# Kernel optimization log

Hardware: AMD Instinct MI355X
Metric: run time of the kernel (lower is better)

The kernel has to match this reference:

```python
import jax, jax.numpy as jnp
import numpy as np

D_MODEL, N_LEVELS, N_HEADS, N_POINTS = 256, 3, 8, 2
HEAD_DIM = D_MODEL // N_HEADS
SPATIAL_SHAPES = np.array([[100, 100], [50, 50], [25, 25]], dtype=np.int32)
LEN_IN = int((SPATIAL_SHAPES[:, 0] * SPATIAL_SHAPES[:, 1]).sum())  # 13125
BS, NQ = 16, 900


def setup_inputs() -> dict:
    key = jax.random.key(0)
    ks = jax.random.split(key, 12)
    s = 1.0 / np.sqrt(D_MODEL)
    return {
        "query": jax.random.normal(ks[0], (BS, NQ, N_LEVELS, D_MODEL), jnp.float32),
        "reference_points": jax.random.uniform(ks[1], (BS, NQ, N_LEVELS, 2), jnp.float32),
        "input_flatten": jax.random.normal(ks[2], (BS, LEN_IN, D_MODEL), jnp.float32),
        "input_spatial_shapes": jnp.asarray(SPATIAL_SHAPES),
        "W_value": jax.random.normal(ks[3], (D_MODEL, D_MODEL), jnp.float32) * s,
        "b_value": jnp.zeros((D_MODEL,), jnp.float32),
        "W_off": jax.random.normal(ks[4], (D_MODEL, N_HEADS * N_LEVELS * N_POINTS * 2), jnp.float32) * s * 0.1,
        "b_off": jax.random.normal(ks[5], (N_HEADS * N_LEVELS * N_POINTS * 2,), jnp.float32) * 0.5,
        "W_attn": jax.random.normal(ks[6], (D_MODEL, N_HEADS * N_LEVELS * N_POINTS), jnp.float32) * s,
        "b_attn": jnp.zeros((N_HEADS * N_LEVELS * N_POINTS,), jnp.float32),
        "W_out": jax.random.normal(ks[7], (D_MODEL, D_MODEL), jnp.float32) * s,
        "b_out": jnp.zeros((D_MODEL,), jnp.float32),
    }


def _bilinear_sample(v, loc, H, W):
    """v: (bs, nh, H*W, hd); loc in [0,1]: (bs, nh, N, 2). Zero-pad out of range."""
    hd = v.shape[-1]
    x = loc[..., 0] * W - 0.5
    y = loc[..., 1] * H - 0.5
    x0 = jnp.floor(x)
    y0 = jnp.floor(y)
    out = jnp.zeros(x.shape + (hd,), v.dtype)
    for dx in (0, 1):
        for dy in (0, 1):
            xi = x0 + dx
            yi = y0 + dy
            wgt = (1.0 - jnp.abs(x - xi)) * (1.0 - jnp.abs(y - yi))
            valid = (xi >= 0) & (xi <= W - 1) & (yi >= 0) & (yi <= H - 1)
            xi_c = jnp.clip(xi, 0, W - 1).astype(jnp.int32)
            yi_c = jnp.clip(yi, 0, H - 1).astype(jnp.int32)
            idx = yi_c * W + xi_c  # (bs, nh, N)
            idx = jnp.broadcast_to(idx[..., None], idx.shape + (hd,))
            g = jnp.take_along_axis(v, idx, axis=2)  # (bs, nh, N, hd)
            out = out + g * (wgt * valid.astype(wgt.dtype))[..., None]
    return out


def reference(query, reference_points, input_flatten, input_spatial_shapes,
              W_value, b_value, W_off, b_off, W_attn, b_attn, W_out, b_out):
    bs, nq, fl, _ = query.shape
    shapes = np.asarray(input_spatial_shapes)  # static pyramid shapes

    # value projection: (bs, Len, nh, hd)
    value = (input_flatten @ W_value + b_value).reshape(bs, -1, N_HEADS, HEAD_DIM)

    # sampling offsets: (bs, nq, fl, nh, nl, np, 2)
    offsets = (query @ W_off + b_off).reshape(bs, nq, fl, N_HEADS, N_LEVELS, N_POINTS, 2)
    # attention weights softmax over (nl*np): (bs, nq, fl, nh, nl, np)
    attn = (query @ W_attn + b_attn).reshape(bs, nq, fl, N_HEADS, N_LEVELS * N_POINTS)
    attn = jax.nn.softmax(attn, axis=-1).reshape(bs, nq, fl, N_HEADS, N_LEVELS, N_POINTS)

    # normalized sampling locations: ref + offset / (W_l, H_l)
    normalizer = jnp.asarray(shapes[:, ::-1], jnp.float32)  # (nl, 2) = (W, H)
    loc = reference_points[:, :, :, None, None, None, :] + offsets / normalizer[None, None, None, None, :, None, :]

    splits = np.cumsum([h * w for h, w in shapes])[:-1]
    value_list = jnp.split(value, splits, axis=1)

    out = jnp.zeros((bs, N_HEADS, nq, fl, HEAD_DIM), value.dtype)
    for lvl, (H, W) in enumerate(shapes):
        H, W = int(H), int(W)
        v = jnp.transpose(value_list[lvl], (0, 2, 1, 3))  # (bs, nh, H*W, hd)
        loc_l = jnp.transpose(loc[:, :, :, :, lvl], (0, 3, 1, 2, 4, 5))  # (bs, nh, nq, fl, np, 2)
        loc_flat = loc_l.reshape(bs, N_HEADS, nq * fl * N_POINTS, 2)
        sampled = _bilinear_sample(v, loc_flat, H, W).reshape(bs, N_HEADS, nq, fl, N_POINTS, HEAD_DIM)
        w = jnp.transpose(attn[:, :, :, :, lvl], (0, 3, 1, 2, 4))  # (bs, nh, nq, fl, np)
        out = out + jnp.einsum("bhqfpd,bhqfp->bhqfd", sampled, w)

    out = jnp.transpose(out, (0, 2, 3, 1, 4)).reshape(bs, nq, fl, D_MODEL)
    return out @ W_out + b_out
```

## Files before the change

### kernel.cpp

```cpp
#include <hip/hip_runtime.h>
#include <math.h>

#define D_MODEL   256
#define N_HEADS   8
#define HEAD_DIM  32
#define N_LEVELS  3
#define N_POINTS  2
#define BS        16
#define NQ        900
#define LEN_IN    13125
#define M_Q       (BS * NQ * N_LEVELS)
#define M_V       (BS * LEN_IN)
#define NCAT      144
#define NCATP     192

typedef _Float16 f16x8 __attribute__((ext_vector_type(8)));
typedef _Float16 f16x4 __attribute__((ext_vector_type(4)));
typedef float f32x4 __attribute__((ext_vector_type(4)));

__global__ __launch_bounds__(256) void convert_weight_kernel(
    const float* __restrict__ W, _Float16* __restrict__ Wth,
    _Float16* __restrict__ Wtl, int N, int Npad) {
  const int idx = blockIdx.x * 256 + threadIdx.x;
  if (idx >= Npad * 256) return;
  const int n = idx >> 8;
  const int k = idx & 255;
  const float v = (n < N) ? W[(size_t)k * N + n] : 0.0f;
  const _Float16 h = (_Float16)v;
  Wth[idx] = h;
  Wtl[idx] = (_Float16)(v - (float)h);
}

__global__ __launch_bounds__(256) void convert_cat_kernel(
    const float* __restrict__ Woff, const float* __restrict__ Wattn,
    const float* __restrict__ boff, const float* __restrict__ battn,
    _Float16* __restrict__ Wth, _Float16* __restrict__ Wtl,
    float* __restrict__ bcat) {
  const int idx = blockIdx.x * 256 + threadIdx.x;
  if (idx >= NCATP * 256) return;
  const int n = idx >> 8;
  const int k = idx & 255;
  float v = 0.0f;
  if (n < 96) v = Woff[(size_t)k * 96 + n];
  else if (n < NCAT) v = Wattn[(size_t)k * 48 + (n - 96)];
  const _Float16 h = (_Float16)v;
  Wth[idx] = h;
  Wtl[idx] = (_Float16)(v - (float)h);
  if (idx < NCAT) bcat[idx] = (idx < 96) ? boff[idx] : battn[idx - 96];
}

template <int FC>
__global__ __launch_bounds__(256) void gemm2_kernel(
    const float* __restrict__ A, const _Float16* __restrict__ Bth,
    const _Float16* __restrict__ Btl, const float* __restrict__ bias,
    float* __restrict__ C, int M, int N) {
  constexpr int K = 256;
  constexpr int LDA = 40;
  __shared__ _Float16 Ah[2][64][LDA];
  __shared__ _Float16 Al[2][64][LDA];

  const int tid = threadIdx.x;
  const int wid = tid >> 6;
  const int lane = tid & 63;
  const int bm = blockIdx.x * 64;
  const int rsel = lane & 15;
  const int khi = (lane >> 4) * 8;

  const int arow = tid >> 3;
  const int ak = (tid & 7) * 4;
  const bool g0 = (bm + arow) < M;
  const bool g1 = (bm + arow + 32) < M;
  const float* ap0 = A + (size_t)(bm + arow) * K + ak;
  const float* ap1 = ap0 + (size_t)32 * K;

  const _Float16* bhp = Bth + (size_t)(wid * FC * 16 + rsel) * K + khi;
  const _Float16* blp = Btl + (size_t)(wid * FC * 16 + rsel) * K + khi;

  f32x4 acc[4][FC];
#pragma unroll
  for (int fr = 0; fr < 4; ++fr)
#pragma unroll
    for (int fc = 0; fc < FC; ++fc) acc[fr][fc] = (f32x4)0.0f;

  const float4 z4 = make_float4(0.f, 0.f, 0.f, 0.f);

  float4 a0 = g0 ? *reinterpret_cast<const float4*>(ap0) : z4;
  float4 a1 = g1 ? *reinterpret_cast<const float4*>(ap1) : z4;
  f16x8 bh[FC], bl[FC];
#pragma unroll
  for (int fc = 0; fc < FC; ++fc) {
    bh[fc] = *reinterpret_cast<const f16x8*>(bhp + (size_t)fc * 16 * K);
    bl[fc] = *reinterpret_cast<const f16x8*>(blp + (size_t)fc * 16 * K);
  }
  {
    f16x4 h0, l0, h1, l1;
    h0[0] = (_Float16)a0.x; l0[0] = (_Float16)(a0.x - (float)h0[0]);
    h0[1] = (_Float16)a0.y; l0[1] = (_Float16)(a0.y - (float)h0[1]);
    h0[2] = (_Float16)a0.z; l0[2] = (_Float16)(a0.z - (float)h0[2]);
    h0[3] = (_Float16)a0.w; l0[3] = (_Float16)(a0.w - (float)h0[3]);
    h1[0] = (_Float16)a1.x; l1[0] = (_Float16)(a1.x - (float)h1[0]);
    h1[1] = (_Float16)a1.y; l1[1] = (_Float16)(a1.y - (float)h1[1]);
    h1[2] = (_Float16)a1.z; l1[2] = (_Float16)(a1.z - (float)h1[2]);
    h1[3] = (_Float16)a1.w; l1[3] = (_Float16)(a1.w - (float)h1[3]);
    *reinterpret_cast<f16x4*>(&Ah[0][arow][ak]) = h0;
    *reinterpret_cast<f16x4*>(&Al[0][arow][ak]) = l0;
    *reinterpret_cast<f16x4*>(&Ah[0][arow + 32][ak]) = h1;
    *reinterpret_cast<f16x4*>(&Al[0][arow + 32][ak]) = l1;
  }
  __syncthreads();

#pragma unroll 2
  for (int s = 0; s < 8; ++s) {
    const int cur = s & 1;
    float4 na0 = z4, na1 = z4;
    f16x8 nbh[FC], nbl[FC];
    if (s < 7) {
      na0 = g0 ? *reinterpret_cast<const float4*>(ap0 + (s + 1) * 32) : z4;
      na1 = g1 ? *reinterpret_cast<const float4*>(ap1 + (s + 1) * 32) : z4;
#pragma unroll
      for (int fc = 0; fc < FC; ++fc) {
        nbh[fc] = *reinterpret_cast<const f16x8*>(
            bhp + (size_t)fc * 16 * K + (s + 1) * 32);
        nbl[fc] = *reinterpret_cast<const f16x8*>(
            blp + (size_t)fc * 16 * K + (s + 1) * 32);
      }
    }
    f16x8 afh[4], afl[4];
#pragma unroll
    for (int fr = 0; fr < 4; ++fr) {
      afh[fr] = *reinterpret_cast<const f16x8*>(&Ah[cur][fr * 16 + rsel][khi]);
      afl[fr] = *reinterpret_cast<const f16x8*>(&Al[cur][fr * 16 + rsel][khi]);
    }
#pragma unroll
    for (int fr = 0; fr < 4; ++fr)
#pragma unroll
      for (int fc = 0; fc < FC; ++fc) {
        acc[fr][fc] = __builtin_amdgcn_mfma_f32_16x16x32_f16(
            afh[fr], bh[fc], acc[fr][fc], 0, 0, 0);
        acc[fr][fc] = __builtin_amdgcn_mfma_f32_16x16x32_f16(
            afh[fr], bl[fc], acc[fr][fc], 0, 0, 0);
        acc[fr][fc] = __builtin_amdgcn_mfma_f32_16x16x32_f16(
            afl[fr], bh[fc], acc[fr][fc], 0, 0, 0);
      }
    if (s < 7) {
      const int nxt = cur ^ 1;
      f16x4 h0, l0, h1, l1;
      h0[0] = (_Float16)na0.x; l0[0] = (_Float16)(na0.x - (float)h0[0]);
      h0[1] = (_Float16)na0.y; l0[1] = (_Float16)(na0.y - (float)h0[1]);
      h0[2] = (_Float16)na0.z; l0[2] = (_Float16)(na0.z - (float)h0[2]);
      h0[3] = (_Float16)na0.w; l0[3] = (_Float16)(na0.w - (float)h0[3]);
      h1[0] = (_Float16)na1.x; l1[0] = (_Float16)(na1.x - (float)h1[0]);
      h1[1] = (_Float16)na1.y; l1[1] = (_Float16)(na1.y - (float)h1[1]);
      h1[2] = (_Float16)na1.z; l1[2] = (_Float16)(na1.z - (float)h1[2]);
      h1[3] = (_Float16)na1.w; l1[3] = (_Float16)(na1.w - (float)h1[3]);
      *reinterpret_cast<f16x4*>(&Ah[nxt][arow][ak]) = h0;
      *reinterpret_cast<f16x4*>(&Al[nxt][arow][ak]) = l0;
      *reinterpret_cast<f16x4*>(&Ah[nxt][arow + 32][ak]) = h1;
      *reinterpret_cast<f16x4*>(&Al[nxt][arow + 32][ak]) = l1;
#pragma unroll
      for (int fc = 0; fc < FC; ++fc) { bh[fc] = nbh[fc]; bl[fc] = nbl[fc]; }
      __syncthreads();
    }
  }

  float bs_[FC];
#pragma unroll
  for (int fc = 0; fc < FC; ++fc) {
    const int col = wid * FC * 16 + fc * 16 + rsel;
    bs_[fc] = (col < N) ? bias[col] : 0.0f;
  }
#pragma unroll
  for (int fr = 0; fr < 4; ++fr)
#pragma unroll
    for (int i = 0; i < 4; ++i) {
      const int row = bm + fr * 16 + (lane >> 4) * 4 + i;
      if (row >= M) continue;
#pragma unroll
      for (int fc = 0; fc < FC; ++fc) {
        const int col = wid * FC * 16 + fc * 16 + rsel;
        if (col < N) C[(size_t)row * N + col] = acc[fr][fc][i] + bs_[fc];
      }
    }
}

__global__ __launch_bounds__(256) void sample_kernel(
    const float* __restrict__ value, const float* __restrict__ refpts,
    const float* __restrict__ offs_attn, float* __restrict__ out_mid) {
  const int row = blockIdx.x;
  const int tid = threadIdx.x;
  const int h = tid >> 5;
  const int d = tid & 31;
  const int b = row / (NQ * N_LEVELS);

  const int LVL_W[3] = {100, 50, 25};
  const int LVL_H[3] = {100, 50, 25};
  const int LVL_BASE[3] = {0, 10000, 12500};

  const float* off_p  = offs_attn + (size_t)row * NCAT + h * 12;
  const float* attn_p = offs_attn + (size_t)row * NCAT + 96 + h * 6;

  float aw[6];
  float mx = -INFINITY;
#pragma unroll
  for (int j = 0; j < 6; ++j) {
    aw[j] = attn_p[j];
    mx = fmaxf(mx, aw[j]);
  }
  float ssum = 0.f;
#pragma unroll
  for (int j = 0; j < 6; ++j) {
    aw[j] = expf(aw[j] - mx);
    ssum += aw[j];
  }
  const float rs = 1.0f / ssum;

  const float rx = refpts[(size_t)row * 2 + 0];
  const float ry = refpts[(size_t)row * 2 + 1];

  const float* vbase = value + (size_t)b * LEN_IN * 256 + h * 32 + d;
  float acc = 0.f;

#pragma unroll
  for (int l = 0; l < N_LEVELS; ++l) {
    const int W = LVL_W[l], base = LVL_BASE[l];
    const float fW = (float)LVL_W[l], fH = (float)LVL_H[l];
#pragma unroll
    for (int p = 0; p < N_POINTS; ++p) {
      const float ox = off_p[(l * 2 + p) * 2 + 0];
      const float oy = off_p[(l * 2 + p) * 2 + 1];
      const float x = (rx + ox / fW) * fW - 0.5f;
      const float y = (ry + oy / fH) * fH - 0.5f;
      const float x0 = floorf(x);
      const float y0 = floorf(y);
      const float wa = aw[l * 2 + p] * rs;
#pragma unroll
      for (int dy = 0; dy < 2; ++dy) {
#pragma unroll
        for (int dx = 0; dx < 2; ++dx) {
          const float xi = x0 + (float)dx;
          const float yi = y0 + (float)dy;
          const float wgt = (1.0f - fabsf(x - xi)) * (1.0f - fabsf(y - yi));
          const bool valid = (xi >= 0.f) && (xi <= fW - 1.f) &&
                             (yi >= 0.f) && (yi <= fH - 1.f);
          const int xic = (int)fminf(fmaxf(xi, 0.f), fW - 1.f);
          const int yic = (int)fminf(fmaxf(yi, 0.f), fH - 1.f);
          const int pos = base + yic * W + xic;
          const float g = vbase[(size_t)pos * 256];
          acc = fmaf(g, valid ? wgt * wa : 0.0f, acc);
        }
      }
    }
  }
  out_mid[(size_t)row * 256 + tid] = acc;
}

extern "C" void kernel_launch(void* const* d_in, const int* in_sizes, int n_in,
                              void* d_out, int out_size, void* d_ws,
                              size_t ws_size, hipStream_t stream) {
  const float* query   = (const float*)d_in[0];
  const float* refpts  = (const float*)d_in[1];
  const float* in_flat = (const float*)d_in[2];
  const float* W_value = (const float*)d_in[4];
  const float* b_value = (const float*)d_in[5];
  const float* W_off   = (const float*)d_in[6];
  const float* b_off   = (const float*)d_in[7];
  const float* W_attn  = (const float*)d_in[8];
  const float* b_attn  = (const float*)d_in[9];
  const float* W_out   = (const float*)d_in[10];
  const float* b_out   = (const float*)d_in[11];
  float* out = (float*)d_out;

  char* ws = (char*)d_ws;
  float* value     = (float*)ws; ws += (size_t)M_V * 256 * sizeof(float);
  float* out_mid   = (float*)ws; ws += (size_t)M_Q * 256 * sizeof(float);
  float* offs_attn = (float*)ws; ws += (size_t)M_Q * NCAT * sizeof(float);
  _Float16* Wvh = (_Float16*)ws; ws += 256 * 256 * sizeof(_Float16);
  _Float16* Wvl = (_Float16*)ws; ws += 256 * 256 * sizeof(_Float16);
  _Float16* Woh = (_Float16*)ws; ws += 256 * 256 * sizeof(_Float16);
  _Float16* Wol = (_Float16*)ws; ws += 256 * 256 * sizeof(_Float16);
  _Float16* Wch = (_Float16*)ws; ws += NCATP * 256 * sizeof(_Float16);
  _Float16* Wcl = (_Float16*)ws; ws += NCATP * 256 * sizeof(_Float16);
  float* bcat   = (float*)ws;    ws += 256 * sizeof(float);

  const dim3 blk(256);

  convert_weight_kernel<<<dim3(256), blk, 0, stream>>>(W_value, Wvh, Wvl, 256, 256);
  convert_weight_kernel<<<dim3(256), blk, 0, stream>>>(W_out,   Woh, Wol, 256, 256);
  convert_cat_kernel<<<dim3(NCATP), blk, 0, stream>>>(W_off, W_attn, b_off, b_attn,
                                                      Wch, Wcl, bcat);

  gemm2_kernel<4><<<dim3((M_V + 63) / 64), blk, 0, stream>>>(
      in_flat, Wvh, Wvl, b_value, value, M_V, 256);

  gemm2_kernel<3><<<dim3((M_Q + 63) / 64), blk, 0, stream>>>(
      query, Wch, Wcl, bcat, offs_attn, M_Q, NCAT);

  sample_kernel<<<dim3(M_Q), blk, 0, stream>>>(value, refpts, offs_attn,
                                               out_mid);

  gemm2_kernel<4><<<dim3((M_Q + 63) / 64), blk, 0, stream>>>(
      out_mid, Woh, Wol, b_out, out, M_Q, 256);
}
```

Measured before the change: 810.6 us.

## Stage full A tile in swizzled LDS and precompute sampling offsets per query

The GEMM now loads the whole 64x256 A tile into XOR-swizzled shared memory once, split into hi/lo fp16 halves. This removes the per-K-step double buffering and barriers but uses 64KB of LDS per block, which lowers occupancy. The sampling kernel now handles one query across all three feature levels per block. A first phase computes the softmax, bilinear byte offsets and weights into shared memory, so the 256 threads no longer repeat that address and weight arithmetic. Each thread then only gathers values and accumulates.

```diff
diff --git a/kernel.cpp b/kernel.cpp
--- a/kernel.cpp
+++ b/kernel.cpp
@@ -50,14 +50,13 @@
 }
 
 template <int FC>
-__global__ __launch_bounds__(256) void gemm2_kernel(
+__global__ __launch_bounds__(256) void gemm3_kernel(
     const float* __restrict__ A, const _Float16* __restrict__ Bth,
     const _Float16* __restrict__ Btl, const float* __restrict__ bias,
     float* __restrict__ C, int M, int N) {
   constexpr int K = 256;
-  constexpr int LDA = 40;
-  __shared__ _Float16 Ah[2][64][LDA];
-  __shared__ _Float16 Al[2][64][LDA];
+  __shared__ _Float16 Ah[64 * 256];
+  __shared__ _Float16 Al[64 * 256];
 
   const int tid = threadIdx.x;
   const int wid = tid >> 6;
@@ -66,12 +65,26 @@
   const int rsel = lane & 15;
   const int khi = (lane >> 4) * 8;
 
-  const int arow = tid >> 3;
-  const int ak = (tid & 7) * 4;
-  const bool g0 = (bm + arow) < M;
-  const bool g1 = (bm + arow + 32) < M;
-  const float* ap0 = A + (size_t)(bm + arow) * K + ak;
-  const float* ap1 = ap0 + (size_t)32 * K;
+  char* AhB = (char*)Ah;
+  char* AlB = (char*)Al;
+
+#pragma unroll
+  for (int it = 0; it < 16; ++it) {
+    const int idx = it * 1024 + tid * 4;
+    const int row = idx >> 8;
+    const int col = idx & 255;
+    float4 v = make_float4(0.f, 0.f, 0.f, 0.f);
+    if (bm + row < M)
+      v = *reinterpret_cast<const float4*>(&A[(size_t)(bm + row) * K + col]);
+    f16x4 h, l;
+    h[0] = (_Float16)v.x; l[0] = (_Float16)(v.x - (float)h[0]);
+    h[1] = (_Float16)v.y; l[1] = (_Float16)(v.y - (float)h[1]);
+    h[2] = (_Float16)v.z; l[2] = (_Float16)(v.z - (float)h[2]);
+    h[3] = (_Float16)v.w; l[3] = (_Float16)(v.w - (float)h[3]);
+    const int byt = row * 512 + ((col * 2) ^ ((row & 7) << 4));
+    *reinterpret_cast<f16x4*>(AhB + byt) = h;
+    *reinterpret_cast<f16x4*>(AlB + byt) = l;
+  }
 
   const _Float16* bhp = Bth + (size_t)(wid * FC * 16 + rsel) * K + khi;
   const _Float16* blp = Btl + (size_t)(wid * FC * 16 + rsel) * K + khi;
@@ -82,41 +95,21 @@
 #pragma unroll
     for (int fc = 0; fc < FC; ++fc) acc[fr][fc] = (f32x4)0.0f;
 
-  const float4 z4 = make_float4(0.f, 0.f, 0.f, 0.f);
-
-  float4 a0 = g0 ? *reinterpret_cast<const float4*>(ap0) : z4;
-  float4 a1 = g1 ? *reinterpret_cast<const float4*>(ap1) : z4;
   f16x8 bh[FC], bl[FC];
 #pragma unroll
   for (int fc = 0; fc < FC; ++fc) {
     bh[fc] = *reinterpret_cast<const f16x8*>(bhp + (size_t)fc * 16 * K);
     bl[fc] = *reinterpret_cast<const f16x8*>(blp + (size_t)fc * 16 * K);
   }
-  {
-    f16x4 h0, l0, h1, l1;
-    h0[0] = (_Float16)a0.x; l0[0] = (_Float16)(a0.x - (float)h0[0]);
-    h0[1] = (_Float16)a0.y; l0[1] = (_Float16)(a0.y - (float)h0[1]);
-    h0[2] = (_Float16)a0.z; l0[2] = (_Float16)(a0.z - (float)h0[2]);
-    h0[3] = (_Float16)a0.w; l0[3] = (_Float16)(a0.w - (float)h0[3]);
-    h1[0] = (_Float16)a1.x; l1[0] = (_Float16)(a1.x - (float)h1[0]);
-    h1[1] = (_Float16)a1.y; l1[1] = (_Float16)(a1.y - (float)h1[1]);
-    h1[2] = (_Float16)a1.z; l1[2] = (_Float16)(a1.z - (float)h1[2]);
-    h1[3] = (_Float16)a1.w; l1[3] = (_Float16)(a1.w - (float)h1[3]);
-    *reinterpret_cast<f16x4*>(&Ah[0][arow][ak]) = h0;
-    *reinterpret_cast<f16x4*>(&Al[0][arow][ak]) = l0;
-    *reinterpret_cast<f16x4*>(&Ah[0][arow + 32][ak]) = h1;
-    *reinterpret_cast<f16x4*>(&Al[0][arow + 32][ak]) = l1;
-  }
+
   __syncthreads();
 
-#pragma unroll 2
+  const int swzx = (rsel & 7) << 4;
+
+#pragma unroll
   for (int s = 0; s < 8; ++s) {
-    const int cur = s & 1;
-    float4 na0 = z4, na1 = z4;
     f16x8 nbh[FC], nbl[FC];
     if (s < 7) {
-      na0 = g0 ? *reinterpret_cast<const float4*>(ap0 + (s + 1) * 32) : z4;
-      na1 = g1 ? *reinterpret_cast<const float4*>(ap1 + (s + 1) * 32) : z4;
 #pragma unroll
       for (int fc = 0; fc < FC; ++fc) {
         nbh[fc] = *reinterpret_cast<const f16x8*>(
@@ -128,8 +121,10 @@
     f16x8 afh[4], afl[4];
 #pragma unroll
     for (int fr = 0; fr < 4; ++fr) {
-      afh[fr] = *reinterpret_cast<const f16x8*>(&Ah[cur][fr * 16 + rsel][khi]);
-      afl[fr] = *reinterpret_cast<const f16x8*>(&Al[cur][fr * 16 + rsel][khi]);
+      const int row = fr * 16 + rsel;
+      const int byt = row * 512 + (((s * 32 + khi) * 2) ^ swzx);
+      afh[fr] = *reinterpret_cast<const f16x8*>(AhB + byt);
+      afl[fr] = *reinterpret_cast<const f16x8*>(AlB + byt);
     }
 #pragma unroll
     for (int fr = 0; fr < 4; ++fr)
@@ -143,23 +138,8 @@
             afl[fr], bh[fc], acc[fr][fc], 0, 0, 0);
       }
     if (s < 7) {
-      const int nxt = cur ^ 1;
-      f16x4 h0, l0, h1, l1;
-      h0[0] = (_Float16)na0.x; l0[0] = (_Float16)(na0.x - (float)h0[0]);
-      h0[1] = (_Float16)na0.y; l0[1] = (_Float16)(na0.y - (float)h0[1]);
-      h0[2] = (_Float16)na0.z; l0[2] = (_Float16)(na0.z - (float)h0[2]);
-      h0[3] = (_Float16)na0.w; l0[3] = (_Float16)(na0.w - (float)h0[3]);
-      h1[0] = (_Float16)na1.x; l1[0] = (_Float16)(na1.x - (float)h1[0]);
-      h1[1] = (_Float16)na1.y; l1[1] = (_Float16)(na1.y - (float)h1[1]);
-      h1[2] = (_Float16)na1.z; l1[2] = (_Float16)(na1.z - (float)h1[2]);
-      h1[3] = (_Float16)na1.w; l1[3] = (_Float16)(na1.w - (float)h1[3]);
-      *reinterpret_cast<f16x4*>(&Ah[nxt][arow][ak]) = h0;
-      *reinterpret_cast<f16x4*>(&Al[nxt][arow][ak]) = l0;
-      *reinterpret_cast<f16x4*>(&Ah[nxt][arow + 32][ak]) = h1;
-      *reinterpret_cast<f16x4*>(&Al[nxt][arow + 32][ak]) = l1;
 #pragma unroll
       for (int fc = 0; fc < FC; ++fc) { bh[fc] = nbh[fc]; bl[fc] = nbl[fc]; }
-      __syncthreads();
     }
   }
 
@@ -183,75 +163,95 @@
     }
 }
 
-__global__ __launch_bounds__(256) void sample_kernel(
+__global__ __launch_bounds__(256) void sample2_kernel(
     const float* __restrict__ value, const float* __restrict__ refpts,
     const float* __restrict__ offs_attn, float* __restrict__ out_mid) {
-  const int row = blockIdx.x;
+  __shared__ int4   s_off[144];
+  __shared__ float4 s_w[144];
+
+  const int bq = blockIdx.x;
+  const int b = bq / NQ;
   const int tid = threadIdx.x;
+
+  if (tid < 144) {
+    const int fl = tid / 48;
+    const int rem = tid - fl * 48;
+    const int h = rem / 6;
+    const int j = rem - h * 6;
+    const int l = j >> 1;
+
+    const int LVL_W[3] = {100, 50, 25};
+    const int LVL_BASE[3] = {0, 10000, 12500};
+    const int W = LVL_W[l];
+    const int base = LVL_BASE[l];
+    const float fW = (float)W, fH = (float)W;
+
+    const int row = bq * 3 + fl;
+    const float* oa = offs_attn + (size_t)row * NCAT;
+
+    float aw[6];
+    float mx = -INFINITY;
+#pragma unroll
+    for (int jj = 0; jj < 6; ++jj) {
+      aw[jj] = oa[96 + h * 6 + jj];
+      mx = fmaxf(mx, aw[jj]);
+    }
+    float ssum = 0.f;
+#pragma unroll
+    for (int jj = 0; jj < 6; ++jj) ssum += expf(aw[jj] - mx);
+    const float wa = expf(aw[j] - mx) / ssum;
+
+    const float rx = refpts[(size_t)row * 2 + 0];
+    const float ry = refpts[(size_t)row * 2 + 1];
+    const float ox = oa[h * 12 + j * 2 + 0];
+    const float oy = oa[h * 12 + j * 2 + 1];
+    const float x = (rx + ox / fW) * fW - 0.5f;
+    const float y = (ry + oy / fH) * fH - 0.5f;
+    const float x0 = floorf(x);
+    const float y0 = floorf(y);
+
+    int offv[4];
+    float wv[4];
+#pragma unroll
+    for (int dy = 0; dy < 2; ++dy)
+#pragma unroll
+      for (int dx = 0; dx < 2; ++dx) {
+        const float xi = x0 + (float)dx;
+        const float yi = y0 + (float)dy;
+        const float wgt = (1.0f - fabsf(x - xi)) * (1.0f - fabsf(y - yi));
+        const bool valid = (xi >= 0.f) && (xi <= fW - 1.f) &&
+                           (yi >= 0.f) && (yi <= fH - 1.f);
+        const int xic = (int)fminf(fmaxf(xi, 0.f), fW - 1.f);
+        const int yic = (int)fminf(fmaxf(yi, 0.f), fH - 1.f);
+        const int pos = base + yic * W + xic;
+        offv[dy * 2 + dx] = pos * 1024;
+        wv[dy * 2 + dx] = valid ? wgt * wa : 0.0f;
+      }
+    s_off[tid] = make_int4(offv[0], offv[1], offv[2], offv[3]);
+    s_w[tid] = make_float4(wv[0], wv[1], wv[2], wv[3]);
+  }
+  __syncthreads();
+
   const int h = tid >> 5;
   const int d = tid & 31;
-  const int b = row / (NQ * N_LEVELS);
-
-  const int LVL_W[3] = {100, 50, 25};
-  const int LVL_H[3] = {100, 50, 25};
-  const int LVL_BASE[3] = {0, 10000, 12500};
-
-  const float* off_p  = offs_attn + (size_t)row * NCAT + h * 12;
-  const float* attn_p = offs_attn + (size_t)row * NCAT + 96 + h * 6;
-
-  float aw[6];
-  float mx = -INFINITY;
-#pragma unroll
-  for (int j = 0; j < 6; ++j) {
-    aw[j] = attn_p[j];
-    mx = fmaxf(mx, aw[j]);
-  }
-  float ssum = 0.f;
-#pragma unroll
-  for (int j = 0; j < 6; ++j) {
-    aw[j] = expf(aw[j] - mx);
-    ssum += aw[j];
-  }
-  const float rs = 1.0f / ssum;
-
-  const float rx = refpts[(size_t)row * 2 + 0];
-  const float ry = refpts[(size_t)row * 2 + 1];
-
-  const float* vbase = value + (size_t)b * LEN_IN * 256 + h * 32 + d;
-  float acc = 0.f;
-
-#pragma unroll
-  for (int l = 0; l < N_LEVELS; ++l) {
-    const int W = LVL_W[l], base = LVL_BASE[l];
-    const float fW = (float)LVL_W[l], fH = (float)LVL_H[l];
-#pragma unroll
-    for (int p = 0; p < N_POINTS; ++p) {
-      const float ox = off_p[(l * 2 + p) * 2 + 0];
-      const float oy = off_p[(l * 2 + p) * 2 + 1];
-      const float x = (rx + ox / fW) * fW - 0.5f;
-      const float y = (ry + oy / fH) * fH - 0.5f;
-      const float x0 = floorf(x);
-      const float y0 = floorf(y);
-      const float wa = aw[l * 2 + p] * rs;
-#pragma unroll
-      for (int dy = 0; dy < 2; ++dy) {
-#pragma unroll
-        for (int dx = 0; dx < 2; ++dx) {
-          const float xi = x0 + (float)dx;
-          const float yi = y0 + (float)dy;
-          const float wgt = (1.0f - fabsf(x - xi)) * (1.0f - fabsf(y - yi));
-          const bool valid = (xi >= 0.f) && (xi <= fW - 1.f) &&
-                             (yi >= 0.f) && (yi <= fH - 1.f);
-          const int xic = (int)fminf(fmaxf(xi, 0.f), fW - 1.f);
-          const int yic = (int)fminf(fmaxf(yi, 0.f), fH - 1.f);
-          const int pos = base + yic * W + xic;
-          const float g = vbase[(size_t)pos * 256];
-          acc = fmaf(g, valid ? wgt * wa : 0.0f, acc);
-        }
-      }
-    }
-  }
-  out_mid[(size_t)row * 256 + tid] = acc;
+  const char* vb = (const char*)value +
+                   ((size_t)b * LEN_IN * 256 + h * 32 + d) * 4;
+
+#pragma unroll
+  for (int fl = 0; fl < 3; ++fl) {
+    float acc = 0.f;
+#pragma unroll
+    for (int j = 0; j < 6; ++j) {
+      const int rec = fl * 48 + h * 6 + j;
+      const int4 o = s_off[rec];
+      const float4 w = s_w[rec];
+      acc = fmaf(w.x, *(const float*)(vb + o.x), acc);
+      acc = fmaf(w.y, *(const float*)(vb + o.y), acc);
+      acc = fmaf(w.z, *(const float*)(vb + o.z), acc);
+      acc = fmaf(w.w, *(const float*)(vb + o.w), acc);
+    }
+    out_mid[((size_t)bq * 3 + fl) * 256 + tid] = acc;
+  }
 }
 
 extern "C" void kernel_launch(void* const* d_in, const int* in_sizes, int n_in,
@@ -289,15 +289,15 @@
   convert_cat_kernel<<<dim3(NCATP), blk, 0, stream>>>(W_off, W_attn, b_off, b_attn,
                                                       Wch, Wcl, bcat);
 
-  gemm2_kernel<4><<<dim3((M_V + 63) / 64), blk, 0, stream>>>(
+  gemm3_kernel<4><<<dim3((M_V + 63) / 64), blk, 0, stream>>>(
       in_flat, Wvh, Wvl, b_value, value, M_V, 256);
 
-  gemm2_kernel<3><<<dim3((M_Q + 63) / 64), blk, 0, stream>>>(
+  gemm3_kernel<3><<<dim3((M_Q + 63) / 64), blk, 0, stream>>>(
       query, Wch, Wcl, bcat, offs_attn, M_Q, NCAT);
 
-  sample_kernel<<<dim3(M_Q), blk, 0, stream>>>(value, refpts, offs_attn,
-                                               out_mid);
-
-  gemm2_kernel<4><<<dim3((M_Q + 63) / 64), blk, 0, stream>>>(
+  sample2_kernel<<<dim3(BS * NQ), blk, 0, stream>>>(value, refpts, offs_attn,
+                                                    out_mid);
+
+  gemm3_kernel<4><<<dim3((M_Q + 63) / 64), blk, 0, stream>>>(
       out_mid, Woh, Wol, b_out, out, M_Q, 256);
 }
```

After: 853.9 us. 1.05x slower.
